# Optimization experiments

Hardware: AMD Instinct MI355X
Metric: run time of the kernel (lower is better)

## Reference

```python
import jax, jax.numpy as jnp
import numpy as np

INPUT_SIZE = 608
STRIDE = 32
NUM_CLASSES = 20
NMS_THRESH = 0.5
NUM_ANCHOR = 5
ANCHORS = np.array([[1.19, 1.98], [2.79, 4.59], [4.53, 8.92], [8.06, 5.29], [10.32, 10.65]], dtype=np.float32)


def _conv(x, w, b, pad):
    # x: NCHW, w: OIHW
    y = jax.lax.conv_general_dilated(x, w, (1, 1), [(pad, pad), (pad, pad)],
                                     dimension_numbers=('NCHW', 'OIHW', 'NCHW'))
    return y + b[None, :, None, None]


def _leaky(x):
    return jnp.where(x > 0, x, 0.1 * x)


def _reorg(x, s=2):
    # space-to-depth, darknet reorg: [B,C,H,W] -> [B,C*s*s,H/s,W/s]
    B, C, H, W = x.shape
    x = x.reshape(B, C, H // s, s, W // s, s)
    x = x.transpose(0, 3, 5, 1, 2, 4)
    return x.reshape(B, C * s * s, H // s, W // s)


def _forward_boxes_scores(feat_layer2, feat_layer3, w1a, b1a, w1b, b1b, wr, br, w2, b2, wp, bp):
    p5 = _leaky(_conv(feat_layer3, w1a, b1a, 1))
    p5 = _leaky(_conv(p5, w1b, b1b, 1))
    p4 = _reorg(_leaky(_conv(feat_layer2, wr, br, 0)))         # [1,256,19,19]
    p5 = jnp.concatenate([p4, p5], axis=1)                      # [1,1280,19,19]
    p5 = _leaky(_conv(p5, w2, b2, 1))
    pred = _conv(p5, wp, bp, 0)                                 # [1,125,19,19]
    B, C, H, W = pred.shape
    pred = pred.transpose(0, 2, 3, 1).reshape(B, H * W, C)
    conf = pred[:, :, :NUM_ANCHOR].reshape(B, H * W * NUM_ANCHOR, 1)
    cls = pred[:, :, NUM_ANCHOR:(1 + NUM_CLASSES) * NUM_ANCHOR].reshape(B, H * W * NUM_ANCHOR, NUM_CLASSES)
    reg = pred[:, :, (1 + NUM_CLASSES) * NUM_ANCHOR:].reshape(B, H * W, NUM_ANCHOR, 4)
    # decode_xywh
    gy, gx = jnp.meshgrid(jnp.arange(H), jnp.arange(W), indexing='ij')
    grid = jnp.stack([gx, gy], axis=-1).astype(pred.dtype).reshape(1, H * W, 1, 2)
    anchor_wh = jnp.asarray(ANCHORS).reshape(1, 1, NUM_ANCHOR, 2)
    xy = jax.nn.sigmoid(reg[..., :2]) + grid
    wh = jnp.exp(reg[..., 2:]) * anchor_wh
    xywh = jnp.concatenate([xy, wh], axis=-1).reshape(B, -1, 4) * STRIDE
    boxes = jnp.concatenate([xywh[..., :2] - 0.5 * xywh[..., 2:],
                             xywh[..., :2] + 0.5 * xywh[..., 2:]], axis=-1)
    boxes = jnp.clip(boxes[0] / INPUT_SIZE, 0.0, 1.0)           # [N,4]
    scores = jax.nn.sigmoid(conf[0]) * jax.nn.softmax(cls[0], axis=-1)  # [N,20]
    return boxes, scores


def _per_class_nms(boxes, scores, class_mask):
    # greedy sequential NMS, faithful to the torch while-loop (suppress iff IoU > thresh)
    N = boxes.shape[0]
    s = jnp.where(class_mask, scores, -jnp.inf)
    order = jnp.argsort(-s)
    b = boxes[order]
    valid = class_mask[order]
    x1, y1, x2, y2 = b[:, 0], b[:, 1], b[:, 2], b[:, 3]
    areas = (x2 - x1) * (y2 - y1)
    iw = jnp.maximum(1e-10, jnp.minimum(x2[:, None], x2[None, :]) - jnp.maximum(x1[:, None], x1[None, :]))
    ih = jnp.maximum(1e-10, jnp.minimum(y2[:, None], y2[None, :]) - jnp.maximum(y1[:, None], y1[None, :]))
    inter = iw * ih
    iou = inter / (areas[:, None] + areas[None, :] - inter)
    upper = jnp.arange(N)[None, :] > jnp.arange(N)[:, None]
    sup_mat = (iou > NMS_THRESH) & upper

    def body(i, state):
        suppressed, keep = state
        cur = valid[i] & jnp.logical_not(suppressed[i])
        keep = keep.at[i].set(cur)
        suppressed = suppressed | (cur & sup_mat[i])
        return suppressed, keep

    _, keep_sorted = jax.lax.fori_loop(0, N, body, (jnp.zeros(N, bool), jnp.zeros(N, bool)))
    return jnp.zeros(N, bool).at[order].set(keep_sorted)


def setup_inputs() -> dict:
    key = jax.random.key(0)
    ks = jax.random.split(key, 8)
    w = lambda k, shape: jax.random.normal(k, shape, jnp.float32) * 0.01
    return {
        'feat_layer2': jax.random.normal(ks[0], (1, 512, 38, 38), jnp.float32),
        'feat_layer3': jax.random.normal(ks[1], (1, 1024, 19, 19), jnp.float32),
        'w1a': w(ks[2], (1024, 1024, 3, 3)), 'b1a': jnp.zeros((1024,), jnp.float32),
        'w1b': w(ks[3], (1024, 1024, 3, 3)), 'b1b': jnp.zeros((1024,), jnp.float32),
        'wr': w(ks[4], (64, 512, 1, 1)), 'br': jnp.zeros((64,), jnp.float32),
        'w2': w(ks[5], (1024, 1280, 3, 3)), 'b2': jnp.zeros((1024,), jnp.float32),
        'wp': w(ks[6], (125, 1024, 1, 1)), 'bp': jnp.zeros((125,), jnp.float32),
    }


def reference(feat_layer2, feat_layer3, w1a, b1a, w1b, b1b, wr, br, w2, b2, wp, bp):
    boxes, scores_full = _forward_boxes_scores(feat_layer2, feat_layer3,
                                               w1a, b1a, w1b, b1b, wr, br, w2, b2, wp, bp)
    cls_inds = jnp.argmax(scores_full, axis=1)                          # [N]
    scores = jnp.take_along_axis(scores_full, cls_inds[:, None], axis=1)[:, 0]
    masks = cls_inds[None, :] == jnp.arange(NUM_CLASSES)[:, None]       # [20,N]
    keeps = jax.vmap(lambda m: _per_class_nms(boxes, scores, m))(masks)
    keep = jnp.any(keeps, axis=0)                                       # [N] bool, fixed-shape mask
    return boxes, scores, cls_inds, keep
```

## Files before the change

### kernel.cpp

```cpp
#include <hip/hip_runtime.h>

typedef _Float16 f16;
typedef _Float16 f16x8 __attribute__((ext_vector_type(8)));
typedef float f32x4 __attribute__((ext_vector_type(4)));

#define N_BOX 1805
#define NPIX 361
#define NCLS 20

__device__ __forceinline__ float leakyf(float x){ return x > 0.f ? x : 0.1f*x; }
__device__ __forceinline__ float sigmoidf_(float x){ return 1.f/(1.f + expf(-x)); }

__global__ void transpose_k(const float* __restrict__ src, float* __restrict__ dst, int R, int C){
  int i = blockIdx.x*256 + threadIdx.x;
  if (i < R*C){ int r = i / C, c = i % C; dst[c*R + r] = src[i]; }
}

__global__ void wprep_k(const float* __restrict__ w, f16* __restrict__ whi, f16* __restrict__ wlo,
                        int Cin, int total){
  int i = blockIdx.x*256 + threadIdx.x;
  if (i >= total) return;
  int co = i / Cin, ci = i - co*Cin;
  const float* src = w + (size_t)i*9;
  int K9 = 9*Cin;
  size_t dbase = (size_t)co*K9 + ci;
  #pragma unroll
  for (int t = 0; t < 9; ++t){
    float v = src[t]*64.f;
    f16 hi = (f16)v;
    f16 lo = (f16)(v - (float)hi);
    whi[dbase + (size_t)t*Cin] = hi;
    wlo[dbase + (size_t)t*Cin] = lo;
  }
}

__global__ void act1prep_k(const float* __restrict__ feat3, f16* __restrict__ ah, f16* __restrict__ al){
  int i = blockIdx.x*256 + threadIdx.x;
  if (i >= NPIX*1024) return;
  int p = i >> 10, c = i & 1023;
  float v = feat3[c*NPIX + p];
  f16 hi = (f16)v; f16 lo = (f16)(v - (float)hi);
  ah[i] = hi; al[i] = lo;
}

__global__ __launch_bounds__(256) void reorg_conv_k(const float* __restrict__ feat2,
    const float* __restrict__ wrT, const float* __restrict__ br,
    f16* __restrict__ cath, f16* __restrict__ catl){
  int c  = threadIdx.x & 63;
  int pq = threadIdx.x >> 6;
  int pix = blockIdx.x*4 + pq;
  int y = pix / 38, x = pix % 38;
  __shared__ float s_in[64][4];
  float acc = br[c];
  for (int cb = 0; cb < 512; cb += 64){
    __syncthreads();
    { int k = threadIdx.x >> 2, pp = threadIdx.x & 3;
      s_in[k][pp] = feat2[(cb + k)*1444 + blockIdx.x*4 + pp]; }
    __syncthreads();
    #pragma unroll
    for (int k = 0; k < 64; ++k)
      acc = fmaf(wrT[(cb+k)*64 + c], s_in[k][pq], acc);
  }
  float v = leakyf(acc);
  int co = ((y & 1)*2 + (x & 1))*64 + c;
  int p = (y>>1)*19 + (x>>1);
  f16 hi = (f16)v; f16 lo = (f16)(v - (float)hi);
  size_t o = (size_t)p*1280 + co;
  cath[o] = hi; catl[o] = lo;
}

__global__ __launch_bounds__(256) void conv_mfma_k(
    const f16* __restrict__ whi, const f16* __restrict__ wlo,
    const f16* __restrict__ ahi, const f16* __restrict__ alo,
    float* __restrict__ part, int Cin, int chunks, int cpt)
{
  const int K9 = 9*Cin;
  int cob = blockIdx.x * 128;
  int px0 = blockIdx.y * 128;
  int ks  = blockIdx.z;
  int kc0 = ks * chunks;
  int tid = threadIdx.x;

  __shared__ f16 sAh[128*32], sAl[128*32], sBh[128*32], sBl[128*32];

  int r = tid >> 1, h = tid & 1;
  int wb0 = ((r*64 + h*32)      ) ^ ((r&7)<<4);
  int wb1 = ((r*64 + h*32 + 16) ) ^ ((r&7)<<4);
  const f16* wArowh = whi + (size_t)(cob + r)*K9 + h*16;
  const f16* wArowl = wlo + (size_t)(cob + r)*K9 + h*16;
  int p = px0 + r;
  int py = p / 19, px = p - py*19;

  int lane = tid & 63, wid = tid >> 6;
  int lrow = lane & 15, lgrp = lane >> 4;
  int wr = wid >> 1, wc = wid & 1;
  int swz = (lrow & 7) << 4;
  int aoff[4], boff[4];
  #pragma unroll
  for (int m = 0; m < 4; ++m){
    int rA = wr*64 + m*16 + lrow;
    aoff[m] = (rA*64 + lgrp*16) ^ swz;
    int rB = wc*64 + m*16 + lrow;
    boff[m] = (rB*64 + lgrp*16) ^ swz;
  }

  f32x4 acc[4][4] = {};

  for (int kc = kc0; kc < kc0 + chunks; ++kc){
    int t = kc / cpt;
    int ci0 = (kc - t*cpt) * 32;
    int dy = t / 3, dx = t - dy*3;
    int yy = py + dy - 1, xx = px + dx - 1;
    bool bvalid = (p < NPIX) && ((unsigned)yy < 19u) && ((unsigned)xx < 19u);

    f16x8 a0 = *(const f16x8*)(wArowh + (size_t)kc*32);
    f16x8 a1 = *(const f16x8*)(wArowh + (size_t)kc*32 + 8);
    f16x8 a2 = *(const f16x8*)(wArowl + (size_t)kc*32);
    f16x8 a3 = *(const f16x8*)(wArowl + (size_t)kc*32 + 8);
    f16x8 b0 = {}, b1 = {}, b2 = {}, b3 = {};
    if (bvalid){
      const f16* bh_src = ahi + (size_t)(yy*19+xx)*Cin + ci0 + h*16;
      const f16* bl_src = alo + (size_t)(yy*19+xx)*Cin + ci0 + h*16;
      b0 = *(const f16x8*)(bh_src);
      b1 = *(const f16x8*)(bh_src + 8);
      b2 = *(const f16x8*)(bl_src);
      b3 = *(const f16x8*)(bl_src + 8);
    }
    __syncthreads();
    *(f16x8*)((char*)sAh + wb0) = a0; *(f16x8*)((char*)sAh + wb1) = a1;
    *(f16x8*)((char*)sAl + wb0) = a2; *(f16x8*)((char*)sAl + wb1) = a3;
    *(f16x8*)((char*)sBh + wb0) = b0; *(f16x8*)((char*)sBh + wb1) = b1;
    *(f16x8*)((char*)sBl + wb0) = b2; *(f16x8*)((char*)sBl + wb1) = b3;
    __syncthreads();

    f16x8 bh[4], bl[4];
    #pragma unroll
    for (int n = 0; n < 4; ++n){
      bh[n] = *(const f16x8*)((char*)sBh + boff[n]);
      bl[n] = *(const f16x8*)((char*)sBl + boff[n]);
    }
    #pragma unroll
    for (int m = 0; m < 4; ++m){
      f16x8 ah = *(const f16x8*)((char*)sAh + aoff[m]);
      f16x8 al = *(const f16x8*)((char*)sAl + aoff[m]);
      #pragma unroll
      for (int n = 0; n < 4; ++n){
        acc[m][n] = __builtin_amdgcn_mfma_f32_16x16x32_f16(ah, bh[n], acc[m][n], 0,0,0);
        acc[m][n] = __builtin_amdgcn_mfma_f32_16x16x32_f16(ah, bl[n], acc[m][n], 0,0,0);
        acc[m][n] = __builtin_amdgcn_mfma_f32_16x16x32_f16(al, bh[n], acc[m][n], 0,0,0);
      }
    }
  }

  #pragma unroll
  for (int m = 0; m < 4; ++m){
    #pragma unroll
    for (int n = 0; n < 4; ++n){
      int pp = px0 + wc*64 + n*16 + lrow;
      if (pp < NPIX){
        int co = cob + wr*64 + m*16 + lgrp*4;
        size_t base = ((size_t)ks*1024 + co)*NPIX + pp;
        part[base          ] = acc[m][n][0];
        part[base +   NPIX ] = acc[m][n][1];
        part[base + 2*NPIX ] = acc[m][n][2];
        part[base + 3*NPIX ] = acc[m][n][3];
      }
    }
  }
}

__global__ void reduce16v_k(const float* __restrict__ part, const float* __restrict__ bias,
                            f16* __restrict__ dhi, f16* __restrict__ dlo,
                            int Cstride, int Coff, int splitk){
  int i = blockIdx.x*256 + threadIdx.x;
  if (i >= 1024*NPIX) return;
  int co = i / NPIX, p = i - co*NPIX;
  float s = 0.f;
  for (int k = 0; k < splitk; ++k) s += part[(size_t)k*1024*NPIX + i];
  float v = leakyf(s*0.015625f + bias[co]);
  f16 hi = (f16)v;
  f16 lo = (f16)(v - (float)hi);
  size_t o = (size_t)p*Cstride + Coff + co;
  dhi[o] = hi; dlo[o] = lo;
}

__global__ __launch_bounds__(256) void pred_conv_k(const f16* __restrict__ a3h, const f16* __restrict__ a3l,
    const float* __restrict__ wpT, const float* __restrict__ bp, float* __restrict__ pred){
  int c = threadIdx.x & 127, ph = threadIdx.x >> 7;
  int pix = blockIdx.x*2 + ph;
  __shared__ float s_in[64][2];
  float acc = 0.f;
  for (int cb = 0; cb < 1024; cb += 64){
    __syncthreads();
    if (threadIdx.x < 128){
      int k = threadIdx.x & 63, pp = threadIdx.x >> 6;
      int px2 = blockIdx.x*2 + pp;
      float v = 0.f;
      if (px2 < NPIX){
        size_t o = (size_t)px2*1024 + cb + k;
        v = (float)a3h[o] + (float)a3l[o];
      }
      s_in[k][pp] = v;
    }
    __syncthreads();
    if (c < 125){
      #pragma unroll
      for (int k = 0; k < 64; ++k)
        acc = fmaf(wpT[(cb+k)*125 + c], s_in[k][ph], acc);
    }
  }
  if (c < 125 && pix < NPIX) pred[c*NPIX + pix] = acc + bp[c];
}

__device__ const float ANCW[5] = {1.19f, 2.79f, 4.53f, 8.06f, 10.32f};
__device__ const float ANCH_[5] = {1.98f, 4.59f, 8.92f, 5.29f, 10.65f};

__global__ void decode_k(const float* __restrict__ pred, float* __restrict__ out,
                         int* __restrict__ cls_i, int* __restrict__ cnt){
  int n = blockIdx.x*256 + threadIdx.x;
  if (blockIdx.x == 0 && threadIdx.x < NCLS) cnt[threadIdx.x] = 0;
  if (n >= N_BOX) return;
  int p = n / 5, a = n % 5;
  float conf = pred[a*NPIX + p];
  float cl[20]; float m = -1e30f;
  #pragma unroll
  for (int k = 0; k < 20; ++k){ cl[k] = pred[(5 + a*20 + k)*NPIX + p]; m = fmaxf(m, cl[k]); }
  float s = 0.f;
  #pragma unroll
  for (int k = 0; k < 20; ++k){ cl[k] = expf(cl[k]-m); s += cl[k]; }
  int bi = 0; float bv = cl[0];
  #pragma unroll
  for (int k = 1; k < 20; ++k) if (cl[k] > bv){ bv = cl[k]; bi = k; }
  float score = sigmoidf_(conf) * (bv / s);
  float tx = pred[(105 + a*4 + 0)*NPIX + p];
  float ty = pred[(105 + a*4 + 1)*NPIX + p];
  float tw = pred[(105 + a*4 + 2)*NPIX + p];
  float th = pred[(105 + a*4 + 3)*NPIX + p];
  float gx = (float)(p % 19), gy = (float)(p / 19);
  float cx = (sigmoidf_(tx) + gx) * 32.f;
  float cy = (sigmoidf_(ty) + gy) * 32.f;
  float bw = expf(tw) * ANCW[a] * 32.f;
  float bh = expf(th) * ANCH_[a] * 32.f;
  float x1 = fminf(fmaxf((cx - 0.5f*bw) / 608.f, 0.f), 1.f);
  float y1 = fminf(fmaxf((cy - 0.5f*bh) / 608.f, 0.f), 1.f);
  float x2 = fminf(fmaxf((cx + 0.5f*bw) / 608.f, 0.f), 1.f);
  float y2 = fminf(fmaxf((cy + 0.5f*bh) / 608.f, 0.f), 1.f);
  out[n*4+0]=x1; out[n*4+1]=y1; out[n*4+2]=x2; out[n*4+3]=y2;
  out[7220 + n]  = score;
  out[9025 + n]  = (float)bi;
  out[10830 + n] = 0.f;
  cls_i[n] = bi;
}

__global__ __launch_bounds__(256) void rank_k(const float* __restrict__ scores,
    const int* __restrict__ cls_i, int* __restrict__ ord, int* __restrict__ cnt){
  __shared__ float s_sc[N_BOX];
  __shared__ short s_cl[N_BOX];
  int tid = threadIdx.x;
  for (int j = tid; j < N_BOX; j += 256){ s_sc[j] = scores[j]; s_cl[j] = (short)cls_i[j]; }
  __syncthreads();
  int wid = tid >> 6, lane = tid & 63;
  int i = blockIdx.x*4 + wid;
  if (i >= N_BOX) return;
  float si = s_sc[i]; short ci = s_cl[i];
  int r = 0;
  for (int j = lane; j < N_BOX; j += 64){
    float sj = s_sc[j];
    r += (int)((s_cl[j] == ci) & ((sj > si) | ((sj == si) & (j < i))));
  }
  #pragma unroll
  for (int o = 32; o; o >>= 1) r += __shfl_down(r, o);
  if (lane == 0){
    ord[ci*N_BOX + r] = i;
    atomicAdd(&cnt[ci], 1);
  }
}

__global__ __launch_bounds__(256) void nms2_k(const float* __restrict__ boxes,
    const int* __restrict__ ord, const int* __restrict__ cnt, float* __restrict__ keep){
  __shared__ float X1[N_BOX], Y1[N_BOX], X2[N_BOX], Y2[N_BOX], AR[N_BOX];
  __shared__ unsigned char SUP[N_BOX];
  __shared__ int IDX[N_BOX];
  int c = blockIdx.x, tid = threadIdx.x;
  int n = cnt[c];
  for (int t = tid; t < n; t += 256){
    int bi = ord[c*N_BOX + t];
    float x1 = boxes[bi*4+0], y1 = boxes[bi*4+1], x2 = boxes[bi*4+2], y2 = boxes[bi*4+3];
    X1[t]=x1; Y1[t]=y1; X2[t]=x2; Y2[t]=y2; AR[t]=(x2-x1)*(y2-y1);
    SUP[t]=0; IDX[t]=bi;
  }
  __syncthreads();
  for (int k = 0; k < n; ++k){
    if (!SUP[k]){
      if (tid == 0) keep[IDX[k]] = 1.f;
      float ax1=X1[k], ay1=Y1[k], ax2=X2[k], ay2=Y2[k], areaA=AR[k];
      for (int j = k+1+tid; j < n; j += 256){
        float iw = fmaxf(1e-10f, fminf(ax2,X2[j]) - fmaxf(ax1,X1[j]));
        float ih = fmaxf(1e-10f, fminf(ay2,Y2[j]) - fmaxf(ay1,Y1[j]));
        float inter = iw*ih;
        float iou = inter / (areaA + AR[j] - inter);
        if (iou > 0.5f) SUP[j] = 1;
      }
    }
    __syncthreads();
  }
}

static inline size_t align256(size_t x){ return (x + 255) & ~(size_t)255; }

extern "C" void kernel_launch(void* const* d_in, const int* in_sizes, int n_in,
                              void* d_out, int out_size, void* d_ws, size_t ws_size,
                              hipStream_t stream){
  const float* feat2 = (const float*)d_in[0];
  const float* feat3 = (const float*)d_in[1];
  const float* w1a = (const float*)d_in[2];
  const float* b1a = (const float*)d_in[3];
  const float* w1b = (const float*)d_in[4];
  const float* b1b = (const float*)d_in[5];
  const float* wr  = (const float*)d_in[6];
  const float* br  = (const float*)d_in[7];
  const float* w2  = (const float*)d_in[8];
  const float* b2  = (const float*)d_in[9];
  const float* wp  = (const float*)d_in[10];
  const float* bp  = (const float*)d_in[11];
  float* out = (float*)d_out;
  char* ws = (char*)d_ws;

  size_t off = 0;
  float* part = (float*)(ws + off); off = align256(off + (size_t)16*1024*NPIX*4);
  f16* wh   = (f16*)(ws + off); off = align256(off + (size_t)1024*1280*9*2);
  f16* wl   = (f16*)(ws + off); off = align256(off + (size_t)1024*1280*9*2);
  f16* a1h  = (f16*)(ws + off); off = align256(off + (size_t)NPIX*1024*2);
  f16* a1l  = (f16*)(ws + off); off = align256(off + (size_t)NPIX*1024*2);
  f16* a2h  = (f16*)(ws + off); off = align256(off + (size_t)NPIX*1024*2);
  f16* a2l  = (f16*)(ws + off); off = align256(off + (size_t)NPIX*1024*2);
  f16* a3h  = (f16*)(ws + off); off = align256(off + (size_t)NPIX*1024*2);
  f16* a3l  = (f16*)(ws + off); off = align256(off + (size_t)NPIX*1024*2);
  f16* cath = (f16*)(ws + off); off = align256(off + (size_t)NPIX*1280*2);
  f16* catl = (f16*)(ws + off); off = align256(off + (size_t)NPIX*1280*2);
  float* pred = (float*)(ws + off); off = align256(off + (size_t)125*NPIX*4);
  float* wrT  = (float*)(ws + off); off = align256(off + (size_t)512*64*4);
  float* wpT  = (float*)(ws + off); off = align256(off + (size_t)1024*125*4);
  int* cls_i  = (int*)(ws + off); off = align256(off + (size_t)N_BOX*4);
  int* ord    = (int*)(ws + off); off = align256(off + (size_t)NCLS*N_BOX*4);
  int* cnt    = (int*)(ws + off); off = align256(off + (size_t)NCLS*4);

  transpose_k<<<(64*512 + 255)/256, 256, 0, stream>>>(wr, wrT, 64, 512);
  transpose_k<<<(125*1024 + 255)/256, 256, 0, stream>>>(wp, wpT, 125, 1024);
  act1prep_k<<<(NPIX*1024 + 255)/256, 256, 0, stream>>>(feat3, a1h, a1l);
  reorg_conv_k<<<361, 256, 0, stream>>>(feat2, wrT, br, cath, catl);

  wprep_k<<<(1024*1024 + 255)/256, 256, 0, stream>>>(w1a, wh, wl, 1024, 1024*1024);
  { dim3 g(8, 3, 16);
    conv_mfma_k<<<g, 256, 0, stream>>>(wh, wl, a1h, a1l, part, 1024, 18, 32); }
  reduce16v_k<<<(1024*NPIX + 255)/256, 256, 0, stream>>>(part, b1a, a2h, a2l, 1024, 0, 16);

  wprep_k<<<(1024*1024 + 255)/256, 256, 0, stream>>>(w1b, wh, wl, 1024, 1024*1024);
  { dim3 g(8, 3, 16);
    conv_mfma_k<<<g, 256, 0, stream>>>(wh, wl, a2h, a2l, part, 1024, 18, 32); }
  reduce16v_k<<<(1024*NPIX + 255)/256, 256, 0, stream>>>(part, b1b, cath, catl, 1280, 256, 16);

  wprep_k<<<(1024*1280 + 255)/256, 256, 0, stream>>>(w2, wh, wl, 1280, 1024*1280);
  { dim3 g(8, 3, 15);
    conv_mfma_k<<<g, 256, 0, stream>>>(wh, wl, cath, catl, part, 1280, 24, 40); }
  reduce16v_k<<<(1024*NPIX + 255)/256, 256, 0, stream>>>(part, b2, a3h, a3l, 1024, 0, 15);

  pred_conv_k<<<181, 256, 0, stream>>>(a3h, a3l, wpT, bp, pred);
  decode_k<<<8, 256, 0, stream>>>(pred, out, cls_i, cnt);
  rank_k<<<(N_BOX + 3)/4, 256, 0, stream>>>(out + 7220, cls_i, ord, cnt);
  nms2_k<<<NCLS, 256, 0, stream>>>(out, ord, cnt, out + 10830);
}
```

Baseline: 320.3 us.

## Replace serial per-box NMS loop with parallel IoU bitmask and single-wave scan

```diff
diff --git a/kernel.cpp b/kernel.cpp
--- a/kernel.cpp
+++ b/kernel.cpp
@@ -7,6 +7,8 @@
 #define N_BOX 1805
 #define NPIX 361
 #define NCLS 20
+#define MCAP 320
+#define GNW 29
 
 __device__ __forceinline__ float leakyf(float x){ return x > 0.f ? x : 0.1f*x; }
 __device__ __forceinline__ float sigmoidf_(float x){ return 1.f/(1.f + expf(-x)); }
@@ -277,32 +279,59 @@
 }
 
 __global__ __launch_bounds__(256) void nms2_k(const float* __restrict__ boxes,
-    const int* __restrict__ ord, const int* __restrict__ cnt, float* __restrict__ keep){
+    const int* __restrict__ ord, const int* __restrict__ cnt, float* __restrict__ keep,
+    unsigned long long* __restrict__ gmask){
   __shared__ float X1[N_BOX], Y1[N_BOX], X2[N_BOX], Y2[N_BOX], AR[N_BOX];
-  __shared__ unsigned char SUP[N_BOX];
   __shared__ int IDX[N_BOX];
+  __shared__ unsigned long long smask[MCAP*(MCAP/64 + 1)];
   int c = blockIdx.x, tid = threadIdx.x;
   int n = cnt[c];
+  if (n <= 0) return;
   for (int t = tid; t < n; t += 256){
     int bi = ord[c*N_BOX + t];
     float x1 = boxes[bi*4+0], y1 = boxes[bi*4+1], x2 = boxes[bi*4+2], y2 = boxes[bi*4+3];
     X1[t]=x1; Y1[t]=y1; X2[t]=x2; Y2[t]=y2; AR[t]=(x2-x1)*(y2-y1);
-    SUP[t]=0; IDX[t]=bi;
+    IDX[t]=bi;
   }
   __syncthreads();
-  for (int k = 0; k < n; ++k){
-    if (!SUP[k]){
-      if (tid == 0) keep[IDX[k]] = 1.f;
-      float ax1=X1[k], ay1=Y1[k], ax2=X2[k], ay2=Y2[k], areaA=AR[k];
-      for (int j = k+1+tid; j < n; j += 256){
-        float iw = fmaxf(1e-10f, fminf(ax2,X2[j]) - fmaxf(ax1,X1[j]));
-        float ih = fmaxf(1e-10f, fminf(ay2,Y2[j]) - fmaxf(ay1,Y1[j]));
-        float inter = iw*ih;
-        float iou = inter / (areaA + AR[j] - inter);
-        if (iou > 0.5f) SUP[j] = 1;
+  int nw = (n + 63) >> 6;
+  bool lds = (n <= MCAP);
+  unsigned long long* rows = lds ? smask : (gmask + (size_t)c*N_BOX*GNW);
+  for (int task = tid; task < n*nw; task += 256){
+    int i = task / nw, w = task - i*nw;
+    float ax1=X1[i], ay1=Y1[i], ax2=X2[i], ay2=Y2[i], areaA=AR[i];
+    unsigned long long bits = 0;
+    int j0 = w << 6;
+    int jb = i+1 > j0 ? i+1 : j0;
+    int je = j0+64 < n ? j0+64 : n;
+    for (int j = jb; j < je; ++j){
+      float iw = fmaxf(1e-10f, fminf(ax2,X2[j]) - fmaxf(ax1,X1[j]));
+      float ih = fmaxf(1e-10f, fminf(ay2,Y2[j]) - fmaxf(ay1,Y1[j]));
+      float inter = iw*ih;
+      float iou = inter / (areaA + AR[j] - inter);
+      bits |= (unsigned long long)(iou > 0.5f) << (j - j0);
+    }
+    rows[(size_t)i*nw + w] = bits;
+  }
+  __syncthreads();
+  if (tid < 64){
+    int lane = tid;
+    unsigned long long S = 0;
+    unsigned long long r0,r1,r2,r3;
+    bool act = lane < nw;
+    r0 = (act && 0 < n) ? rows[lane] : 0ull;
+    r1 = (act && 1 < n) ? rows[(size_t)1*nw + lane] : 0ull;
+    r2 = (act && 2 < n) ? rows[(size_t)2*nw + lane] : 0ull;
+    r3 = (act && 3 < n) ? rows[(size_t)3*nw + lane] : 0ull;
+    for (int i = 0; i < n; ++i){
+      unsigned long long row = r0; r0 = r1; r1 = r2; r2 = r3;
+      r3 = (act && i+4 < n) ? rows[(size_t)(i+4)*nw + lane] : 0ull;
+      unsigned long long Siw = __shfl(S, i >> 6);
+      if (!((Siw >> (i & 63)) & 1ull)){
+        if (lane == 0) keep[IDX[i]] = 1.f;
+        S |= row;
       }
     }
-    __syncthreads();
   }
 }
 
@@ -344,6 +373,7 @@
   int* cls_i  = (int*)(ws + off); off = align256(off + (size_t)N_BOX*4);
   int* ord    = (int*)(ws + off); off = align256(off + (size_t)NCLS*N_BOX*4);
   int* cnt    = (int*)(ws + off); off = align256(off + (size_t)NCLS*4);
+  unsigned long long* gmask = (unsigned long long*)part;
 
   transpose_k<<<(64*512 + 255)/256, 256, 0, stream>>>(wr, wrT, 64, 512);
   transpose_k<<<(125*1024 + 255)/256, 256, 0, stream>>>(wp, wpT, 125, 1024);
@@ -368,5 +398,5 @@
   pred_conv_k<<<181, 256, 0, stream>>>(a3h, a3l, wpT, bp, pred);
   decode_k<<<8, 256, 0, stream>>>(pred, out, cls_i, cnt);
   rank_k<<<(N_BOX + 3)/4, 256, 0, stream>>>(out + 7220, cls_i, ord, cnt);
-  nms2_k<<<NCLS, 256, 0, stream>>>(out, ord, cnt, out + 10830);
-}
+  nms2_k<<<NCLS, 256, 0, stream>>>(out, ord, cnt, out + 10830, gmask);
+}
```

Result: slower. 340.6 us (+6.3%).
